# Kernel tuning notes

Hardware: AMD Instinct MI355X
Metric: run time of the kernel (lower is better)

## Reference

```python
import jax, jax.numpy as jnp
import numpy as np

N, IN_DIM, OUT_DIM = 50000, 256, 64
K, DELTA_D = 8, 8            # k = out_dim // (ndim // init_k) = 64 // (64 // 8)
M = 1638400                  # edges
ROUTIT, TAU = 4, 1.0
EPS = 1e-12                  # F.normalize eps


def _l2norm(v, n, k, dd):
    # F.normalize over last dim of (n, k, dd) view, flattened back to (n, k*dd)
    v = v.reshape(n, k, dd)
    nrm = jnp.sqrt(jnp.sum(v * v, axis=2, keepdims=True))
    v = v / jnp.maximum(nrm, EPS)
    return v.reshape(n, k * dd)


def setup_inputs() -> dict:
    key = jax.random.key(0)
    k1, k2, k3, k4 = jax.random.split(key, 4)
    x = jax.random.normal(k1, (N, IN_DIM), dtype=jnp.float32)
    src_trg = jax.random.randint(k2, (2, M), 0, N, dtype=jnp.int64)
    std = 1.0 / np.sqrt(OUT_DIM)
    weight = jax.random.uniform(k3, (IN_DIM, OUT_DIM), dtype=jnp.float32, minval=-std, maxval=std)
    bias = jax.random.uniform(k4, (OUT_DIM,), dtype=jnp.float32, minval=-std, maxval=std)
    return {"x": x, "src_trg": src_trg, "weight": weight, "bias": bias}


def reference(x, src_trg, weight, bias):
    trg, src = src_trg[0], src_trg[1]
    n = x.shape[0]
    d = K * DELTA_D
    # DimReduceLayer + leaky_relu + per-capsule L2 normalize
    h = jax.nn.leaky_relu(x @ weight + bias)          # (n, d)
    h = _l2norm(h, n, K, DELTA_D)
    # RoutingLayer normalizes again (idempotent up to eps, kept for fidelity)
    h = _l2norm(h, n, K, DELTA_D)
    z = h[src].reshape(M, K, DELTA_D)                  # gather source capsules
    c = h
    for _ in range(ROUTIT):
        ct = c[trg].reshape(M, K, DELTA_D)             # gather target capsules
        p = jnp.sum(z * ct, axis=2)                    # (m, k) per-edge capsule scores
        p = jax.nn.softmax(p / TAU, axis=1)
        ws = (p[:, :, None] * z).reshape(M, d)         # weighted messages
        c = c.at[trg].add(ws)                          # scatter-add into targets
        c = _l2norm(c, n, K, DELTA_D)
    return c
```

## Files before the change

kernel.cpp:

```cpp
#include <hip/hip_runtime.h>
#include <math.h>
#include <stdint.h>

#define IN_DIM 256
#define OUT_D 64
#define ROUTIT 4
#define LCAP 48
#define NG 6
#define BSH 7
#define NBMAX 512

typedef float v2f __attribute__((ext_vector_type(2)));
__device__ __forceinline__ v2f pk_fma(v2f a, v2f b, v2f c) {
    return __builtin_elementwise_fma(a, b, c);
}

__device__ __forceinline__ float dpp_add_xor1(float x) {
    return x + __int_as_float(__builtin_amdgcn_mov_dpp(__float_as_int(x), 0xB1, 0xF, 0xF, true));
}
__device__ __forceinline__ float dpp_add_xor2(float x) {
    return x + __int_as_float(__builtin_amdgcn_mov_dpp(__float_as_int(x), 0x4E, 0xF, 0xF, true));
}
__device__ __forceinline__ float dpp_add_xor8(float x) {
    return x + __int_as_float(__builtin_amdgcn_mov_dpp(__float_as_int(x), 0x128, 0xF, 0xF, true));
}
__device__ __forceinline__ float swz_add_xor4(float x) {
    return x + __int_as_float(__builtin_amdgcn_ds_swizzle(__float_as_int(x), 0x101F));
}
__device__ __forceinline__ float swz_add_xor16(float x) {
    return x + __int_as_float(__builtin_amdgcn_ds_swizzle(__float_as_int(x), 0x401F));
}

__device__ __forceinline__ void load8p(v2f z[4], const float* p) {
    float4 a = *(const float4*)p;
    float4 b = *(const float4*)(p + 4);
    z[0] = (v2f){a.x, a.y}; z[1] = (v2f){a.z, a.w};
    z[2] = (v2f){b.x, b.y}; z[3] = (v2f){b.z, b.w};
}

__global__ __launch_bounds__(512, 2) void gemm_norm_kernel(
    const float* __restrict__ x, const float* __restrict__ w,
    const float* __restrict__ bias, float* __restrict__ h, int n)
{
    __shared__ float wlds[IN_DIM * OUT_D];
    {
        const float4* wsrc = (const float4*)w;
        float4* wdst = (float4*)wlds;
        #pragma unroll
        for (int i = 0; i < (IN_DIM * OUT_D / 4); i += 512)
            wdst[i + threadIdx.x] = wsrc[i + threadIdx.x];
    }
    __syncthreads();

    int lane = threadIdx.x & 63;
    int wv   = threadIdx.x >> 6;
    int c0   = wv * 8;
    int base = blockIdx.x * 256;

    const float* xr[4];
    int rows[4];
    #pragma unroll
    for (int r = 0; r < 4; ++r) {
        rows[r] = base + r * 64 + lane;
        int rc = rows[r] < n ? rows[r] : n - 1;
        xr[r] = x + (size_t)rc * IN_DIM;
    }

    v2f b2[4];
    #pragma unroll
    for (int j = 0; j < 4; ++j) b2[j] = (v2f){bias[c0 + 2*j], bias[c0 + 2*j + 1]};
    v2f acc[4][4];
    #pragma unroll
    for (int r = 0; r < 4; ++r)
        #pragma unroll
        for (int j = 0; j < 4; ++j) acc[r][j] = b2[j];

    float4 xa[4], xb[4];
    #pragma unroll
    for (int r = 0; r < 4; ++r) {
        xa[r] = *(const float4*)(xr[r]);
        xb[r] = *(const float4*)(xr[r] + 4);
    }

    for (int k0 = 0; k0 < IN_DIM; k0 += 8) {
        int kn = (k0 + 8 < IN_DIM) ? k0 + 8 : 0;
        float4 na[4], nb[4];
        #pragma unroll
        for (int r = 0; r < 4; ++r) {
            na[r] = *(const float4*)(xr[r] + kn);
            nb[r] = *(const float4*)(xr[r] + kn + 4);
        }
        const float* wk = wlds + k0 * OUT_D + c0;
        #pragma unroll
        for (int kk = 0; kk < 8; ++kk) {
            float4 w0 = *(const float4*)(wk + kk * OUT_D);
            float4 w1 = *(const float4*)(wk + kk * OUT_D + 4);
            v2f wvp[4] = {{w0.x,w0.y},{w0.z,w0.w},{w1.x,w1.y},{w1.z,w1.w}};
            #pragma unroll
            for (int r = 0; r < 4; ++r) {
                float xs = (kk < 4)
                    ? ((kk == 0) ? xa[r].x : (kk == 1) ? xa[r].y : (kk == 2) ? xa[r].z : xa[r].w)
                    : ((kk == 4) ? xb[r].x : (kk == 5) ? xb[r].y : (kk == 6) ? xb[r].z : xb[r].w);
                v2f xs2 = (v2f){xs, xs};
                acc[r][0] = pk_fma(xs2, wvp[0], acc[r][0]);
                acc[r][1] = pk_fma(xs2, wvp[1], acc[r][1]);
                acc[r][2] = pk_fma(xs2, wvp[2], acc[r][2]);
                acc[r][3] = pk_fma(xs2, wvp[3], acc[r][3]);
            }
        }
        #pragma unroll
        for (int r = 0; r < 4; ++r) { xa[r] = na[r]; xb[r] = nb[r]; }
    }

    #pragma unroll
    for (int r = 0; r < 4; ++r) {
        if (rows[r] < n) {
            float a[8];
            #pragma unroll
            for (int j = 0; j < 4; ++j) { a[2*j] = acc[r][j][0]; a[2*j+1] = acc[r][j][1]; }
            #pragma unroll
            for (int c = 0; c < 8; ++c) a[c] = a[c] > 0.0f ? a[c] : 0.01f * a[c];
            #pragma unroll
            for (int rep = 0; rep < 2; ++rep) {
                float ss = 0.0f;
                #pragma unroll
                for (int d = 0; d < 8; ++d) ss = fmaf(a[d], a[d], ss);
                float inv = 1.0f / fmaxf(sqrtf(ss), 1e-12f);
                #pragma unroll
                for (int d = 0; d < 8; ++d) a[d] *= inv;
            }
            float* hr = h + (size_t)rows[r] * OUT_D + c0;
            float4 o1, o2;
            o1.x=a[0]; o1.y=a[1]; o1.z=a[2]; o1.w=a[3];
            o2.x=a[4]; o2.y=a[5]; o2.z=a[6]; o2.w=a[7];
            *(float4*)hr = o1;
            *(float4*)(hr + 4) = o2;
        }
    }
}


__global__ __launch_bounds__(256) void bucket_hist_kernel(
    const int* __restrict__ trg, int m4, int* __restrict__ bucket_counts, int nb)
{
    __shared__ int hist[NBMAX];
    for (int i = threadIdx.x; i < nb; i += 256) hist[i] = 0;
    __syncthreads();
    for (int i = blockIdx.x * 256 + threadIdx.x; i < m4; i += 256 * gridDim.x) {
        int4 t = ((const int4*)trg)[i];
        atomicAdd(&hist[t.x >> BSH], 1);
        atomicAdd(&hist[t.y >> BSH], 1);
        atomicAdd(&hist[t.z >> BSH], 1);
        atomicAdd(&hist[t.w >> BSH], 1);
    }
    __syncthreads();
    for (int i = threadIdx.x; i < nb; i += 256) {
        int c = hist[i];
        if (c) atomicAdd(&bucket_counts[i], c);
    }
}

__global__ __launch_bounds__(64) void bucket_scan_kernel(
    const int* __restrict__ bucket_counts, int* __restrict__ bucket_base,
    int* __restrict__ bucket_cursor, int nb, int n, int m, int* __restrict__ row_start)
{
    int lane = threadIdx.x;
    int carry = 0;
    for (int base = 0; base <= nb; base += 64) {
        int i = base + lane;
        int v = (i < nb) ? bucket_counts[i] : 0;
        int s = v;
        #pragma unroll
        for (int off = 1; off < 64; off <<= 1) {
            int t = __shfl_up(s, off, 64);
            if (lane >= off) s += t;
        }
        if (i <= nb) {
            int exc = carry + s - v;
            bucket_base[i]   = exc;
            bucket_cursor[i] = exc;
        }
        carry += __shfl(s, 63, 64);
    }
    if (lane == 0) row_start[n] = m;
}

__global__ __launch_bounds__(1024) void partition_kernel(
    const int* __restrict__ trg, const int* __restrict__ src, int m4,
    uint32_t* __restrict__ epack, int* __restrict__ bucket_cursor, int nb)
{
    __shared__ int hist[NBMAX];
    __shared__ int runbase[NBMAX];
    for (int i = threadIdx.x; i < nb; i += 1024) hist[i] = 0;
    __syncthreads();
    int base4 = blockIdx.x * 2048;
    #pragma unroll
    for (int j = 0; j < 2; ++j) {
        int i4 = base4 + j * 1024 + threadIdx.x;
        if (i4 < m4) {
            int4 t = ((const int4*)trg)[i4];
            atomicAdd(&hist[t.x >> BSH], 1);
            atomicAdd(&hist[t.y >> BSH], 1);
            atomicAdd(&hist[t.z >> BSH], 1);
            atomicAdd(&hist[t.w >> BSH], 1);
        }
    }
    __syncthreads();
    for (int i = threadIdx.x; i < nb; i += 1024) {
        int c = hist[i];
        runbase[i] = c ? atomicAdd(&bucket_cursor[i], c) : 0;
    }
    __syncthreads();
    for (int i = threadIdx.x; i < nb; i += 1024) hist[i] = 0;
    __syncthreads();
    #pragma unroll
    for (int j = 0; j < 2; ++j) {
        int i4 = base4 + j * 1024 + threadIdx.x;
        if (i4 < m4) {
            int4 t = ((const int4*)trg)[i4];
            int4 s = ((const int4*)src)[i4];
            int tt[4] = {t.x, t.y, t.z, t.w};
            int ss[4] = {s.x, s.y, s.z, s.w};
            #pragma unroll
            for (int q = 0; q < 4; ++q) {
                int b = tt[q] >> BSH;
                int r = atomicAdd(&hist[b], 1);
                epack[runbase[b] + r] =
                    ((uint32_t)(tt[q] & ((1 << BSH) - 1)) << 16) | (uint32_t)ss[q];
            }
        }
    }
}

__global__ __launch_bounds__(512) void local_csr_kernel(
    const uint32_t* __restrict__ epack, const int* __restrict__ bucket_base,
    int* __restrict__ row_start, int* __restrict__ edge_src, int n)
{
    __shared__ int hist[128];
    __shared__ int excl[129];
    __shared__ int cursor[128];
    int b = blockIdx.x;
    int ebeg = bucket_base[b], eend = bucket_base[b + 1];
    int node0 = b << BSH;
    if (threadIdx.x < 128) hist[threadIdx.x] = 0;
    __syncthreads();
    for (int e = ebeg + (int)threadIdx.x; e < eend; e += 512)
        atomicAdd(&hist[epack[e] >> 16], 1);
    __syncthreads();
    if (threadIdx.x < 64) {
        int lane = threadIdx.x;
        int carry = 0;
        #pragma unroll
        for (int c = 0; c < 2; ++c) {
            int i = c * 64 + lane;
            int v = hist[i];
            int s = v;
            #pragma unroll
            for (int off = 1; off < 64; off <<= 1) {
                int t = __shfl_up(s, off, 64);
                if (lane >= off) s += t;
            }
            excl[i] = carry + s - v;
            carry += __shfl(s, 63, 64);
        }
        if (lane == 0) excl[128] = carry;
    }
    __syncthreads();
    int nh = n - node0; if (nh > 128) nh = 128;
    for (int i = threadIdx.x; i <= nh; i += 512)
        row_start[node0 + i] = ebeg + excl[i];
    if (threadIdx.x < 128) cursor[threadIdx.x] = excl[threadIdx.x];
    __syncthreads();
    for (int e = ebeg + (int)threadIdx.x; e < eend; e += 512) {
        uint32_t p = epack[e];
        int r = atomicAdd(&cursor[p >> 16], 1);
        edge_src[ebeg + r] = (int)(p & 0xFFFFu);
    }
}

__device__ __forceinline__ void route_group(const v2f z[4], const v2f c[4], v2f acc[4]) {
    v2f p2 = z[0] * c[0];
    p2 = pk_fma(z[1], c[1], p2);
    p2 = pk_fma(z[2], c[2], p2);
    p2 = pk_fma(z[3], c[3], p2);
    float p = p2[0] + p2[1];
    float ex = __expf(p);
    float sm = dpp_add_xor1(ex);
    sm = dpp_add_xor2(sm);
    sm = dpp_add_xor8(sm);
    float wgt = __fdividef(ex, sm);
    v2f w2 = (v2f){wgt, wgt};
    acc[0] = pk_fma(w2, z[0], acc[0]);
    acc[1] = pk_fma(w2, z[1], acc[1]);
    acc[2] = pk_fma(w2, z[2], acc[2]);
    acc[3] = pk_fma(w2, z[3], acc[3]);
}

__global__ __launch_bounds__(256, 4) void route_kernel(
    const float* __restrict__ h, const int* __restrict__ row_start,
    const int* __restrict__ edge_src, float* __restrict__ out, int n)
{
    int lane = threadIdx.x & 63;
    int wid  = threadIdx.x >> 6;
    int v = blockIdx.x * 4 + wid;
    if (v >= n) return;
    int beg = row_start[v];
    int deg = row_start[v + 1] - beg;
    int nl  = deg < LCAP ? deg : LCAP;
    int ngroups = (nl + 7) >> 3;

    int k  = (lane & 3) | ((lane >> 1) & 4);
    int eo = ((lane >> 2) & 1) | ((lane >> 3) & 6);

    v2f c[4];
    load8p(c, h + (size_t)v * OUT_D + k * 8);

    v2f z[NG][4];
    #pragma unroll
    for (int g = 0; g < NG; ++g) {
        int e = g * 8 + eo;
        if (e < nl) {
            int s = edge_src[beg + e];
            load8p(z[g], h + (size_t)s * OUT_D + k * 8);
        } else {
            #pragma unroll
            for (int d = 0; d < 4; ++d) z[g][d] = (v2f){0.0f, 0.0f};
        }
    }

    #pragma unroll
    for (int it = 0; it < ROUTIT; ++it) {
        v2f acc[4] = {{0,0},{0,0},{0,0},{0,0}};
        #pragma unroll
        for (int g = 0; g < NG; ++g)
            if (g < ngroups) route_group(z[g], c, acc);
        if (deg > LCAP) {
            for (int e0 = LCAP; e0 < deg; e0 += 8) {
                int e = e0 + eo;
                v2f zt[4] = {{0,0},{0,0},{0,0},{0,0}};
                if (e < deg) {
                    int s = edge_src[beg + e];
                    load8p(zt, h + (size_t)s * OUT_D + k * 8);
                }
                route_group(zt, c, acc);
            }
        }
        float ss = 0.0f;
        #pragma unroll
        for (int d = 0; d < 8; ++d) {
            float a = acc[d >> 1][d & 1];
            a = swz_add_xor4(a);
            a = swz_add_xor16(a);
            a += __shfl_xor(a, 32, 64);
            float cv = c[d >> 1][d & 1] + a;
            c[d >> 1][d & 1] = cv;
            ss = fmaf(cv, cv, ss);
        }
        float inv = 1.0f / fmaxf(sqrtf(ss), 1e-12f);
        v2f inv2 = (v2f){inv, inv};
        #pragma unroll
        for (int j = 0; j < 4; ++j) c[j] *= inv2;
    }
    if (eo == 0) {
        float* op = out + (size_t)v * OUT_D + k * 8;
        float4 o1, o2;
        o1.x=c[0][0]; o1.y=c[0][1]; o1.z=c[1][0]; o1.w=c[1][1];
        o2.x=c[2][0]; o2.y=c[2][1]; o2.z=c[3][0]; o2.w=c[3][1];
        *(float4*)op = o1;
        *(float4*)(op + 4) = o2;
    }
}

extern "C" void kernel_launch(void* const* d_in, const int* in_sizes, int n_in,
                              void* d_out, int out_size, void* d_ws, size_t ws_size,
                              hipStream_t stream)
{
    const float* x       = (const float*)d_in[0];
    const int*   src_trg = (const int*)d_in[1];
    const float* w       = (const float*)d_in[2];
    const float* bias    = (const float*)d_in[3];
    float*       out     = (float*)d_out;

    int n = in_sizes[0] / IN_DIM;
    int m = in_sizes[1] / 2;
    int m4 = m >> 2;
    int nb = (n + 127) >> BSH;
    const int* trg = src_trg;
    const int* src = src_trg + m;

    char* wsb = (char*)d_ws;
    size_t off = 0;
    float*    h        = (float*)(wsb + off);    off += (size_t)n * OUT_D * sizeof(float);
    int*      rowstart = (int*)(wsb + off);      off += (size_t)(n + 1) * sizeof(int);
    off = (off + 255) & ~(size_t)255;
    int*      edgesrc  = (int*)(wsb + off);      off += (size_t)m * sizeof(int);
    off = (off + 255) & ~(size_t)255;
    uint32_t* epack    = (uint32_t*)(wsb + off); off += (size_t)m * sizeof(uint32_t);
    int*      bcounts  = (int*)(wsb + off);      off += (size_t)(nb + 1) * sizeof(int);
    int*      bbase    = (int*)(wsb + off);      off += (size_t)(nb + 1) * sizeof(int);
    int*      bcursor  = (int*)(wsb + off);      off += (size_t)(nb + 1) * sizeof(int);

    hipMemsetAsync(bcounts, 0, (size_t)(nb + 1) * sizeof(int), stream);
    gemm_norm_kernel<<<(n + 255) / 256, 512, 0, stream>>>(x, w, bias, h, n);
    bucket_hist_kernel<<<256, 256, 0, stream>>>(trg, m4, bcounts, nb);
    bucket_scan_kernel<<<1, 64, 0, stream>>>(bcounts, bbase, bcursor, nb, n, m, rowstart);
    partition_kernel<<<(m4 + 2047) / 2048, 1024, 0, stream>>>(trg, src, m4, epack, bcursor, nb);
    local_csr_kernel<<<nb, 512, 0, stream>>>(epack, bbase, rowstart, edgesrc, n);
    route_kernel<<<(n + 3) / 4, 256, 0, stream>>>(h, rowstart, edgesrc, out, n);
}
```

Measured before the change: 280.4 us.

## Stage partition and local CSR scatters in shared memory for coalesced writes

The partition kernel now processes 8192 edges per block. It computes a block-local prefix scan of the bucket histogram, scatters edges into an LDS staging buffer in bucket order, and then writes them out contiguously using per-bucket global offsets. The local CSR kernel likewise sorts source indices into an LDS buffer of 6144 entries before a linear write-back, and falls back to direct global writes past that capacity. The goal is to replace random global scatter writes with mostly coalesced ones. The cost is more LDS per block (32KB in partition), which lowers occupancy, plus the extra scan and sync work.

Result: faster. 273.2 us (-2.6%).

```diff
diff --git a/kernel.cpp b/kernel.cpp
--- a/kernel.cpp
+++ b/kernel.cpp
@@ -9,6 +9,8 @@
 #define NG 6
 #define BSH 7
 #define NBMAX 512
+#define PEDGES 8192
+#define LCCAP 6144
 
 typedef float v2f __attribute__((ext_vector_type(2)));
 __device__ __forceinline__ v2f pk_fma(v2f a, v2f b, v2f c) {
@@ -189,13 +191,15 @@
     const int* __restrict__ trg, const int* __restrict__ src, int m4,
     uint32_t* __restrict__ epack, int* __restrict__ bucket_cursor, int nb)
 {
+    __shared__ uint32_t stage[PEDGES];
     __shared__ int hist[NBMAX];
-    __shared__ int runbase[NBMAX];
+    __shared__ int lbase[NBMAX];
+    __shared__ int gdelta[NBMAX];
     for (int i = threadIdx.x; i < nb; i += 1024) hist[i] = 0;
     __syncthreads();
-    int base4 = blockIdx.x * 2048;
-    #pragma unroll
-    for (int j = 0; j < 2; ++j) {
+    int base4 = blockIdx.x * (PEDGES / 4);
+    #pragma unroll
+    for (int j = 0; j < PEDGES / 4 / 1024; ++j) {
         int i4 = base4 + j * 1024 + threadIdx.x;
         if (i4 < m4) {
             int4 t = ((const int4*)trg)[i4];
@@ -206,15 +210,33 @@
         }
     }
     __syncthreads();
+    if (threadIdx.x < 64) {
+        int lane = threadIdx.x;
+        int carry = 0;
+        for (int b0 = 0; b0 < nb; b0 += 64) {
+            int i = b0 + lane;
+            int v = (i < nb) ? hist[i] : 0;
+            int s = v;
+            #pragma unroll
+            for (int off = 1; off < 64; off <<= 1) {
+                int t = __shfl_up(s, off, 64);
+                if (lane >= off) s += t;
+            }
+            if (i < nb) lbase[i] = carry + s - v;
+            carry += __shfl(s, 63, 64);
+        }
+    }
+    __syncthreads();
     for (int i = threadIdx.x; i < nb; i += 1024) {
         int c = hist[i];
-        runbase[i] = c ? atomicAdd(&bucket_cursor[i], c) : 0;
+        int g = c ? atomicAdd(&bucket_cursor[i], c) : 0;
+        gdelta[i] = g - lbase[i];
     }
     __syncthreads();
     for (int i = threadIdx.x; i < nb; i += 1024) hist[i] = 0;
     __syncthreads();
     #pragma unroll
-    for (int j = 0; j < 2; ++j) {
+    for (int j = 0; j < PEDGES / 4 / 1024; ++j) {
         int i4 = base4 + j * 1024 + threadIdx.x;
         if (i4 < m4) {
             int4 t = ((const int4*)trg)[i4];
@@ -225,10 +247,17 @@
             for (int q = 0; q < 4; ++q) {
                 int b = tt[q] >> BSH;
                 int r = atomicAdd(&hist[b], 1);
-                epack[runbase[b] + r] =
-                    ((uint32_t)(tt[q] & ((1 << BSH) - 1)) << 16) | (uint32_t)ss[q];
-            }
-        }
+                stage[lbase[b] + r] = ((uint32_t)tt[q] << 16) | (uint32_t)ss[q];
+            }
+        }
+    }
+    __syncthreads();
+    int rem = (m4 - base4) * 4;
+    int cnt = rem < PEDGES ? rem : PEDGES;
+    for (int i = threadIdx.x; i < cnt; i += 1024) {
+        uint32_t p = stage[i];
+        int b = (int)(p >> (16 + BSH));
+        epack[gdelta[b] + i] = p;
     }
 }
 
@@ -236,16 +265,18 @@
     const uint32_t* __restrict__ epack, const int* __restrict__ bucket_base,
     int* __restrict__ row_start, int* __restrict__ edge_src, int n)
 {
+    __shared__ int sorted[LCCAP];
     __shared__ int hist[128];
     __shared__ int excl[129];
     __shared__ int cursor[128];
     int b = blockIdx.x;
     int ebeg = bucket_base[b], eend = bucket_base[b + 1];
+    int cnt = eend - ebeg;
     int node0 = b << BSH;
     if (threadIdx.x < 128) hist[threadIdx.x] = 0;
     __syncthreads();
-    for (int e = ebeg + (int)threadIdx.x; e < eend; e += 512)
-        atomicAdd(&hist[epack[e] >> 16], 1);
+    for (int e = threadIdx.x; e < cnt; e += 512)
+        atomicAdd(&hist[(epack[ebeg + e] >> 16) & 127], 1);
     __syncthreads();
     if (threadIdx.x < 64) {
         int lane = threadIdx.x;
@@ -271,11 +302,17 @@
         row_start[node0 + i] = ebeg + excl[i];
     if (threadIdx.x < 128) cursor[threadIdx.x] = excl[threadIdx.x];
     __syncthreads();
-    for (int e = ebeg + (int)threadIdx.x; e < eend; e += 512) {
-        uint32_t p = epack[e];
-        int r = atomicAdd(&cursor[p >> 16], 1);
-        edge_src[ebeg + r] = (int)(p & 0xFFFFu);
-    }
+    for (int e = threadIdx.x; e < cnt; e += 512) {
+        uint32_t p = epack[ebeg + e];
+        int r = atomicAdd(&cursor[(p >> 16) & 127], 1);
+        int sv = (int)(p & 0xFFFFu);
+        if (r < LCCAP) sorted[r] = sv;
+        else edge_src[ebeg + r] = sv;
+    }
+    __syncthreads();
+    int lim = cnt < LCCAP ? cnt : LCCAP;
+    for (int i = threadIdx.x; i < lim; i += 512)
+        edge_src[ebeg + i] = sorted[i];
 }
 
 __device__ __forceinline__ void route_group(const v2f z[4], const v2f c[4], v2f acc[4]) {
@@ -404,7 +441,7 @@
     gemm_norm_kernel<<<(n + 255) / 256, 512, 0, stream>>>(x, w, bias, h, n);
     bucket_hist_kernel<<<256, 256, 0, stream>>>(trg, m4, bcounts, nb);
     bucket_scan_kernel<<<1, 64, 0, stream>>>(bcounts, bbase, bcursor, nb, n, m, rowstart);
-    partition_kernel<<<(m4 + 2047) / 2048, 1024, 0, stream>>>(trg, src, m4, epack, bcursor, nb);
+    partition_kernel<<<(m + PEDGES - 1) / PEDGES, 1024, 0, stream>>>(trg, src, m4, epack, bcursor, nb);
     local_csr_kernel<<<nb, 512, 0, stream>>>(epack, bbase, rowstart, edgesrc, n);
     route_kernel<<<(n + 3) / 4, 256, 0, stream>>>(h, rowstart, edgesrc, out, n);
 }
```
